# Performance work log

Hardware: AMD Instinct MI355X
Metric: run time of the kernel (lower is better)

Reference implementation:

```python
import jax, jax.numpy as jnp
import numpy as np

N_HEADS = 16
NEG_INF = -1e9


def setup_inputs() -> dict:
    key = jax.random.key(0)
    k1, k2, k3 = jax.random.split(key, 3)
    B, S, D = 4, 4096, 1024
    x = jax.random.normal(k1, (B, S, D), dtype=jnp.float32)
    # GPT-2-style init scale
    w_qkv = jax.random.normal(k2, (D, 3 * D), dtype=jnp.float32) * 0.02
    b_qkv = jnp.zeros((3 * D,), dtype=jnp.float32)
    w_o = jax.random.normal(k3, (D, D), dtype=jnp.float32) * 0.02
    b_o = jnp.zeros((D,), dtype=jnp.float32)
    return {"x": x, "w_qkv": w_qkv, "b_qkv": b_qkv, "w_o": w_o, "b_o": b_o,
            "window_size": 512}


def reference(x, w_qkv, b_qkv, w_o, b_o, window_size):
    B, S, D = x.shape
    W = window_size
    n_win = S // W  # loop `for i in range(0, S, W)` with S % W == 0
    H = N_HEADS
    dh = D // H

    # All windows are independent -> fold them into the batch dim instead of a
    # Python loop (same math as looping + concat along seq dim).
    xw = x.reshape(B * n_win, W, D)

    qkv = xw @ w_qkv + b_qkv                      # [BN, W, 3D]
    q, k, v = jnp.split(qkv, 3, axis=-1)
    # [BN, H, W, dh]
    q = q.reshape(-1, W, H, dh).transpose(0, 2, 1, 3)
    k = k.reshape(-1, W, H, dh).transpose(0, 2, 1, 3)
    v = v.reshape(-1, W, H, dh).transpose(0, 2, 1, 3)

    scale = 1.0 / jnp.sqrt(jnp.asarray(dh, dtype=x.dtype))
    scores = jnp.einsum('bhqd,bhkd->bhqk', q, k) * scale  # [BN, H, W, W]
    causal = jnp.tril(jnp.ones((W, W), dtype=bool))       # GPT-2 causal mask (per window)
    scores = jnp.where(causal, scores, NEG_INF)
    attn = jax.nn.softmax(scores, axis=-1)

    out = jnp.einsum('bhqk,bhkd->bhqd', attn, v)          # [BN, H, W, dh]
    out = out.transpose(0, 2, 1, 3).reshape(-1, W, D)     # [BN, W, D]
    out = out @ w_o + b_o
    return out.reshape(B, S, D)
```

## Files before the change

kernel.cpp:

```cpp
#include <hip/hip_runtime.h>


typedef unsigned short u16;
typedef unsigned int u32;
typedef __attribute__((ext_vector_type(8))) short bf16x8;
typedef __attribute__((ext_vector_type(4))) float f32x4;

__device__ __forceinline__ float bf2f(u16 v) {
  union { u32 u; float f; } t; t.u = ((u32)v) << 16; return t.f;
}
__device__ __forceinline__ u16 f2bf(float f) {
  union { float f; u32 u; } t; t.f = f;
  u32 u = t.u + 0x7fffu + ((t.u >> 16) & 1u);
  return (u16)(u >> 16);
}
__device__ __forceinline__ void g2lds16(const void* g, void* l) {
  __builtin_amdgcn_global_load_lds((const __attribute__((address_space(1))) void*)g,
                                   (__attribute__((address_space(3))) void*)l,
                                   16, 0, 0);
}

__global__ __launch_bounds__(256) void canon_x(
    const float* __restrict__ xf, u16* __restrict__ xb) {
  size_t i = ((size_t)blockIdx.x * 256 + threadIdx.x) * 8;
  float4 a = *(const float4*)(xf + i);
  float4 b = *(const float4*)(xf + i + 4);
  u16 o[8] = { f2bf(a.x), f2bf(a.y), f2bf(a.z), f2bf(a.w),
               f2bf(b.x), f2bf(b.y), f2bf(b.z), f2bf(b.w) };
  *(bf16x8*)(xb + i) = *(bf16x8*)o;
}

__global__ __launch_bounds__(256) void transpose_w(
    const float* __restrict__ in, u16* __restrict__ out, int R, int C) {
  __shared__ u16 tile[32][33];
  int c0 = blockIdx.x * 32, r0 = blockIdx.y * 32;
  int tx = threadIdx.x & 31, ty = threadIdx.x >> 5;
#pragma unroll
  for (int i = 0; i < 32; i += 8)
    tile[ty + i][tx] = f2bf(in[(size_t)(r0 + ty + i) * C + c0 + tx]);
  __syncthreads();
#pragma unroll
  for (int i = 0; i < 32; i += 8)
    out[(size_t)(c0 + ty + i) * R + r0 + tx] = tile[tx][ty + i];
}

__global__ __launch_bounds__(256) void transpose_v(
    const u16* __restrict__ qkv, u16* __restrict__ vt) {
  __shared__ u16 tile[32][33];
  int bh = blockIdx.z, bn = bh >> 4, h = bh & 15;
  int t0 = blockIdx.x * 32, d0 = blockIdx.y * 32;
  int tx = threadIdx.x & 31, ty = threadIdx.x >> 5;
  const u16* src = qkv + (size_t)(bn * 512) * 3072 + 2048 + h * 64;
#pragma unroll
  for (int i = 0; i < 32; i += 8)
    tile[ty + i][tx] = src[(size_t)(t0 + ty + i) * 3072 + d0 + tx];
  __syncthreads();
  u16* dst = vt + ((size_t)bh * 64 + d0) * 512 + t0;
#pragma unroll
  for (int i = 0; i < 32; i += 8)
    dst[(size_t)(ty + i) * 512 + tx] = tile[tx][ty + i];
}

template <typename OutT>
__global__ __launch_bounds__(256, 2) void gemm_bt_bias(
    const u16* __restrict__ A, const u16* __restrict__ Bt,
    const float* __restrict__ bias, OutT* __restrict__ C,
    int M, int N, int K) {
  __shared__ __align__(16) u16 As[128 * 32];
  __shared__ __align__(16) u16 Bs[128 * 32];
  const int tid = threadIdx.x;
  const int wave = tid >> 6, lane = tid & 63;
  const int quad = lane >> 4, l16 = lane & 15;
  const int m0 = blockIdx.y * 128, n0 = blockIdx.x * 128;
  const int wm = (wave >> 1) * 64, wn = (wave & 1) * 64;

  f32x4 acc[4][4] = {};

  int e0 = (wave * 512) + lane * 8;
  int e1 = 2048 + e0;
  int rA0 = e0 >> 5, cA0 = e0 & 31;
  int rA1 = e1 >> 5, cA1 = e1 & 31;
  const u16* ga0 = A + (size_t)(m0 + rA0) * K + cA0;
  const u16* ga1 = A + (size_t)(m0 + rA1) * K + cA1;
  const u16* gb0 = Bt + (size_t)(n0 + rA0) * K + cA0;
  const u16* gb1 = Bt + (size_t)(n0 + rA1) * K + cA1;
  u16* As0 = As + (size_t)wave * 512;
  u16* As1 = As0 + 2048;
  u16* Bs0 = Bs + (size_t)wave * 512;
  u16* Bs1 = Bs0 + 2048;

  for (int k0 = 0; k0 < K; k0 += 32) {
    g2lds16(ga0 + k0, As0);
    g2lds16(ga1 + k0, As1);
    g2lds16(gb0 + k0, Bs0);
    g2lds16(gb1 + k0, Bs1);
    __syncthreads();
    bf16x8 a[4], b[4];
#pragma unroll
    for (int mi = 0; mi < 4; ++mi)
      a[mi] = *(const bf16x8*)(As + (wm + mi * 16 + l16) * 32 + quad * 8);
#pragma unroll
    for (int ni = 0; ni < 4; ++ni)
      b[ni] = *(const bf16x8*)(Bs + (wn + ni * 16 + l16) * 32 + quad * 8);
#pragma unroll
    for (int mi = 0; mi < 4; ++mi)
#pragma unroll
      for (int ni = 0; ni < 4; ++ni)
        acc[mi][ni] = __builtin_amdgcn_mfma_f32_16x16x32_bf16(a[mi], b[ni], acc[mi][ni], 0, 0, 0);
    __syncthreads();
  }

#pragma unroll
  for (int ni = 0; ni < 4; ++ni) {
    int col = n0 + wn + ni * 16 + l16;
    float bv = bias[col];
#pragma unroll
    for (int mi = 0; mi < 4; ++mi) {
      int row = m0 + wm + mi * 16 + quad * 4;
#pragma unroll
      for (int r = 0; r < 4; ++r) {
        float v = acc[mi][ni][r] + bv;
        if constexpr (sizeof(OutT) == 2)
          C[(size_t)(row + r) * N + col] = f2bf(v);
        else
          C[(size_t)(row + r) * N + col] = v;
      }
    }
  }
}

__global__ __launch_bounds__(256, 2) void attn_win(
    const u16* __restrict__ qkv, const u16* __restrict__ vt,
    u16* __restrict__ attn) {
  __shared__ __align__(16) u16 Qs[128 * 64];
  __shared__ __align__(16) u16 Ks[128 * 64];
  __shared__ __align__(16) u16 Vs[64 * 128];
  __shared__ __align__(16) u16 Ps[4][32 * 128];

  const int qt = blockIdx.x, h = blockIdx.y, bn = blockIdx.z;
  const int bh = bn * 16 + h;
  const int tid = threadIdx.x;
  const int wave = tid >> 6, lane = tid & 63;
  const int quad = lane >> 4, l16 = lane & 15;
  const int t0 = bn * 512 + qt * 128;

#pragma unroll
  for (int it = 0; it < 4; ++it) {
    int i = it * 256 + tid;
    int row = i >> 3, c = i & 7;
    bf16x8 v = *(const bf16x8*)(qkv + (size_t)(t0 + row) * 3072 + h * 64 + c * 8);
    *(bf16x8*)(Qs + row * 64 + ((c ^ (row & 7)) * 8)) = v;
  }

  float mrun[2][4], lrun[2][4];
  f32x4 o[2][4] = {};
#pragma unroll
  for (int mi = 0; mi < 2; ++mi)
#pragma unroll
    for (int r = 0; r < 4; ++r) { mrun[mi][r] = -1e30f; lrun[mi][r] = 0.f; }

  const float cexp = 0.18033688011112042f;

  for (int j = 0; j <= qt; ++j) {
    int tk = bn * 512 + j * 128;
#pragma unroll
    for (int it = 0; it < 4; ++it) {
      int i = it * 256 + tid;
      int rk = i >> 3, ck = i & 7;
      bf16x8 kv = *(const bf16x8*)(qkv + (size_t)(tk + rk) * 3072 + 1024 + h * 64 + ck * 8);
      *(bf16x8*)(Ks + rk * 64 + ((ck ^ (rk & 7)) * 8)) = kv;
      int rv = i >> 4, cv = i & 15;
      bf16x8 vv = *(const bf16x8*)(vt + ((size_t)bh * 64 + rv) * 512 + j * 128 + cv * 8);
      *(bf16x8*)(Vs + rv * 128 + ((cv ^ (rv & 15)) * 8)) = vv;
    }
    __syncthreads();

    f32x4 s[2][8] = {};
#pragma unroll
    for (int ks = 0; ks < 2; ++ks) {
      bf16x8 aq[2];
#pragma unroll
      for (int mi = 0; mi < 2; ++mi) {
        int m = wave * 32 + mi * 16 + l16;
        aq[mi] = *(const bf16x8*)(Qs + m * 64 + (((ks * 4 + quad) ^ (m & 7)) * 8));
      }
#pragma unroll
      for (int ni = 0; ni < 8; ++ni) {
        int n = ni * 16 + l16;
        bf16x8 bk = *(const bf16x8*)(Ks + n * 64 + (((ks * 4 + quad) ^ (n & 7)) * 8));
        s[0][ni] = __builtin_amdgcn_mfma_f32_16x16x32_bf16(aq[0], bk, s[0][ni], 0, 0, 0);
        s[1][ni] = __builtin_amdgcn_mfma_f32_16x16x32_bf16(aq[1], bk, s[1][ni], 0, 0, 0);
      }
    }

    const bool diag = (j == qt);
#pragma unroll
    for (int mi = 0; mi < 2; ++mi) {
#pragma unroll
      for (int r = 0; r < 4; ++r) {
        int m = wave * 32 + mi * 16 + quad * 4 + r;
        float rmax = -1e30f;
#pragma unroll
        for (int ni = 0; ni < 8; ++ni) {
          float v = s[mi][ni][r] * cexp;
          if (diag && (ni * 16 + l16 > m)) v = -1e30f;
          s[mi][ni][r] = v;
          rmax = fmaxf(rmax, v);
        }
        rmax = fmaxf(rmax, __shfl_xor(rmax, 1));
        rmax = fmaxf(rmax, __shfl_xor(rmax, 2));
        rmax = fmaxf(rmax, __shfl_xor(rmax, 4));
        rmax = fmaxf(rmax, __shfl_xor(rmax, 8));
        float mnew = fmaxf(mrun[mi][r], rmax);
        float alpha = exp2f(mrun[mi][r] - mnew);
        mrun[mi][r] = mnew;
        float rsum = 0.f;
#pragma unroll
        for (int ni = 0; ni < 8; ++ni) {
          float pv = exp2f(s[mi][ni][r] - mnew);
          s[mi][ni][r] = pv;
          rsum += pv;
        }
        rsum += __shfl_xor(rsum, 1);
        rsum += __shfl_xor(rsum, 2);
        rsum += __shfl_xor(rsum, 4);
        rsum += __shfl_xor(rsum, 8);
        lrun[mi][r] = lrun[mi][r] * alpha + rsum;
#pragma unroll
        for (int di = 0; di < 4; ++di) o[mi][di][r] *= alpha;
      }
    }

    u16* pw = &Ps[wave][0];
#pragma unroll
    for (int mi = 0; mi < 2; ++mi)
#pragma unroll
      for (int ni = 0; ni < 8; ++ni)
#pragma unroll
        for (int r = 0; r < 4; ++r) {
          int row = mi * 16 + quad * 4 + r;
          int col = ni * 16 + l16;
          int phys = (col >> 3) ^ (row & 15);
          pw[row * 128 + phys * 8 + (col & 7)] = f2bf(s[mi][ni][r]);
        }
    __syncthreads();

#pragma unroll
    for (int ks = 0; ks < 4; ++ks) {
      bf16x8 ap[2];
#pragma unroll
      for (int mi = 0; mi < 2; ++mi) {
        int row = mi * 16 + l16;
        ap[mi] = *(const bf16x8*)(pw + row * 128 + (((ks * 4 + quad) ^ (row & 15)) * 8));
      }
#pragma unroll
      for (int di = 0; di < 4; ++di) {
        int n = di * 16 + l16;
        bf16x8 bv = *(const bf16x8*)(Vs + n * 128 + (((ks * 4 + quad) ^ (n & 15)) * 8));
        o[0][di] = __builtin_amdgcn_mfma_f32_16x16x32_bf16(ap[0], bv, o[0][di], 0, 0, 0);
        o[1][di] = __builtin_amdgcn_mfma_f32_16x16x32_bf16(ap[1], bv, o[1][di], 0, 0, 0);
      }
    }
    __syncthreads();
  }

#pragma unroll
  for (int mi = 0; mi < 2; ++mi)
#pragma unroll
    for (int r = 0; r < 4; ++r) {
      float inv = 1.0f / lrun[mi][r];
      int trow = t0 + wave * 32 + mi * 16 + quad * 4 + r;
#pragma unroll
      for (int di = 0; di < 4; ++di)
        attn[(size_t)trow * 1024 + h * 64 + di * 16 + l16] = f2bf(o[mi][di][r] * inv);
    }
}

extern "C" void kernel_launch(void* const* d_in, const int* in_sizes, int n_in,
                              void* d_out, int out_size, void* d_ws, size_t ws_size,
                              hipStream_t stream) {
  (void)in_sizes; (void)n_in; (void)out_size; (void)ws_size;
  const float* x     = (const float*)d_in[0];
  const float* w_qkv = (const float*)d_in[1];
  const float* b_qkv = (const float*)d_in[2];
  const float* w_o   = (const float*)d_in[3];
  const float* b_o   = (const float*)d_in[4];
  float* out = (float*)d_out;

  char* ws = (char*)d_ws;
  u16* qkv   = (u16*)(ws + 0);
  u16* vtb   = (u16*)(ws + 100663296);
  u16* attnb = (u16*)(ws + 134217728);
  u16* xb    = (u16*)(ws + 167772160);
  u16* wqkvT = (u16*)(ws + 201326592);
  u16* woT   = (u16*)(ws + 207618048);

  canon_x<<<8192, 256, 0, stream>>>(x, xb);
  transpose_w<<<dim3(96, 32), 256, 0, stream>>>(w_qkv, wqkvT, 1024, 3072);
  transpose_w<<<dim3(32, 32), 256, 0, stream>>>(w_o, woT, 1024, 1024);

  gemm_bt_bias<u16><<<dim3(24, 128), 256, 0, stream>>>(
      xb, wqkvT, b_qkv, qkv, 16384, 3072, 1024);
  transpose_v<<<dim3(16, 2, 512), 256, 0, stream>>>(qkv, vtb);
  attn_win<<<dim3(4, 16, 32), 256, 0, stream>>>(qkv, vtb, attnb);
  gemm_bt_bias<float><<<dim3(8, 128), 256, 0, stream>>>(
      attnb, woT, b_o, out, 16384, 1024, 1024);
}
```

Baseline: 468.3 us.

## Load attention Q/K/V operands straight from global into registers, dropping LDS staging

The windowed attention kernel no longer stages Q, K and V tiles in shared memory. Each wave loads its Q fragments into registers once and reads K and V MFMA operands directly from global memory on every step. Because only the per-wave P buffer stays in LDS, the block-wide barriers are removed. The smaller LDS footprint lets the launch bound rise to 3 blocks per CU, and s_setprio is raised around the MFMA loops. In exchange, every wave re-fetches the same K/V tiles, which multiplies L2/global traffic and exposes load latency next to the MFMAs.

```diff
diff --git a/kernel.cpp b/kernel.cpp
--- a/kernel.cpp
+++ b/kernel.cpp
@@ -129,12 +129,9 @@
   }
 }
 
-__global__ __launch_bounds__(256, 2) void attn_win(
+__global__ __launch_bounds__(256, 3) void attn_win(
     const u16* __restrict__ qkv, const u16* __restrict__ vt,
     u16* __restrict__ attn) {
-  __shared__ __align__(16) u16 Qs[128 * 64];
-  __shared__ __align__(16) u16 Ks[128 * 64];
-  __shared__ __align__(16) u16 Vs[64 * 128];
   __shared__ __align__(16) u16 Ps[4][32 * 128];
 
   const int qt = blockIdx.x, h = blockIdx.y, bn = blockIdx.z;
@@ -144,13 +141,13 @@
   const int quad = lane >> 4, l16 = lane & 15;
   const int t0 = bn * 512 + qt * 128;
 
-#pragma unroll
-  for (int it = 0; it < 4; ++it) {
-    int i = it * 256 + tid;
-    int row = i >> 3, c = i & 7;
-    bf16x8 v = *(const bf16x8*)(qkv + (size_t)(t0 + row) * 3072 + h * 64 + c * 8);
-    *(bf16x8*)(Qs + row * 64 + ((c ^ (row & 7)) * 8)) = v;
-  }
+  bf16x8 aq[2][2];
+#pragma unroll
+  for (int mi = 0; mi < 2; ++mi)
+#pragma unroll
+    for (int ks = 0; ks < 2; ++ks)
+      aq[mi][ks] = *(const bf16x8*)(
+          qkv + (size_t)(t0 + wave * 32 + mi * 16 + l16) * 3072 + h * 64 + ks * 32 + quad * 8);
 
   float mrun[2][4], lrun[2][4];
   f32x4 o[2][4] = {};
@@ -161,37 +158,26 @@
 
   const float cexp = 0.18033688011112042f;
 
+  const u16* Kb = qkv + 1024 + h * 64;
+  const u16* Vb = vt + (size_t)bh * 64 * 512;
+  u16* pw = &Ps[wave][0];
+
   for (int j = 0; j <= qt; ++j) {
-    int tk = bn * 512 + j * 128;
-#pragma unroll
-    for (int it = 0; it < 4; ++it) {
-      int i = it * 256 + tid;
-      int rk = i >> 3, ck = i & 7;
-      bf16x8 kv = *(const bf16x8*)(qkv + (size_t)(tk + rk) * 3072 + 1024 + h * 64 + ck * 8);
-      *(bf16x8*)(Ks + rk * 64 + ((ck ^ (rk & 7)) * 8)) = kv;
-      int rv = i >> 4, cv = i & 15;
-      bf16x8 vv = *(const bf16x8*)(vt + ((size_t)bh * 64 + rv) * 512 + j * 128 + cv * 8);
-      *(bf16x8*)(Vs + rv * 128 + ((cv ^ (rv & 15)) * 8)) = vv;
-    }
-    __syncthreads();
+    const int tk = bn * 512 + j * 128;
 
     f32x4 s[2][8] = {};
+    __builtin_amdgcn_s_setprio(1);
 #pragma unroll
     for (int ks = 0; ks < 2; ++ks) {
-      bf16x8 aq[2];
-#pragma unroll
-      for (int mi = 0; mi < 2; ++mi) {
-        int m = wave * 32 + mi * 16 + l16;
-        aq[mi] = *(const bf16x8*)(Qs + m * 64 + (((ks * 4 + quad) ^ (m & 7)) * 8));
-      }
 #pragma unroll
       for (int ni = 0; ni < 8; ++ni) {
-        int n = ni * 16 + l16;
-        bf16x8 bk = *(const bf16x8*)(Ks + n * 64 + (((ks * 4 + quad) ^ (n & 7)) * 8));
-        s[0][ni] = __builtin_amdgcn_mfma_f32_16x16x32_bf16(aq[0], bk, s[0][ni], 0, 0, 0);
-        s[1][ni] = __builtin_amdgcn_mfma_f32_16x16x32_bf16(aq[1], bk, s[1][ni], 0, 0, 0);
-      }
-    }
+        bf16x8 bk = *(const bf16x8*)(
+            Kb + (size_t)(tk + ni * 16 + l16) * 3072 + ks * 32 + quad * 8);
+        s[0][ni] = __builtin_amdgcn_mfma_f32_16x16x32_bf16(aq[0][ks], bk, s[0][ni], 0, 0, 0);
+        s[1][ni] = __builtin_amdgcn_mfma_f32_16x16x32_bf16(aq[1][ks], bk, s[1][ni], 0, 0, 0);
+      }
+    }
+    __builtin_amdgcn_s_setprio(0);
 
     const bool diag = (j == qt);
 #pragma unroll
@@ -231,7 +217,6 @@
       }
     }
 
-    u16* pw = &Ps[wave][0];
 #pragma unroll
     for (int mi = 0; mi < 2; ++mi)
 #pragma unroll
@@ -243,8 +228,8 @@
           int phys = (col >> 3) ^ (row & 15);
           pw[row * 128 + phys * 8 + (col & 7)] = f2bf(s[mi][ni][r]);
         }
-    __syncthreads();
-
+
+    __builtin_amdgcn_s_setprio(1);
 #pragma unroll
     for (int ks = 0; ks < 4; ++ks) {
       bf16x8 ap[2];
@@ -255,13 +240,13 @@
       }
 #pragma unroll
       for (int di = 0; di < 4; ++di) {
-        int n = di * 16 + l16;
-        bf16x8 bv = *(const bf16x8*)(Vs + n * 128 + (((ks * 4 + quad) ^ (n & 15)) * 8));
+        bf16x8 bv = *(const bf16x8*)(
+            Vb + (size_t)(di * 16 + l16) * 512 + j * 128 + ks * 32 + quad * 8);
         o[0][di] = __builtin_amdgcn_mfma_f32_16x16x32_bf16(ap[0], bv, o[0][di], 0, 0, 0);
         o[1][di] = __builtin_amdgcn_mfma_f32_16x16x32_bf16(ap[1], bv, o[1][di], 0, 0, 0);
       }
     }
-    __syncthreads();
+    __builtin_amdgcn_s_setprio(0);
   }
 
 #pragma unroll
```

After: 683.8 us. 1.46x slower.

## Keep Q in registers, prefetch next K/V tile, halve P buffer for occupancy

Applied to the files above, without the earlier changes.

The attention kernel now loads Q fragments straight into registers instead of staging them through shared memory. It prefetches the next K/V tile into registers while the PV MFMAs of the current tile run, then writes that tile to LDS between two barriers. The P staging buffer is halved by processing the two 16-row halves one after the other, and launch bounds are raised to 3 blocks per CU. s_setprio raises wave priority around the MFMA sections. The extra register pressure from holding Q, K and V in registers may cause spills or block the higher occupancy target.

```diff
diff --git a/kernel.cpp b/kernel.cpp
--- a/kernel.cpp
+++ b/kernel.cpp
@@ -129,13 +129,12 @@
   }
 }
 
-__global__ __launch_bounds__(256, 2) void attn_win(
+__global__ __launch_bounds__(256, 3) void attn_win(
     const u16* __restrict__ qkv, const u16* __restrict__ vt,
     u16* __restrict__ attn) {
-  __shared__ __align__(16) u16 Qs[128 * 64];
   __shared__ __align__(16) u16 Ks[128 * 64];
   __shared__ __align__(16) u16 Vs[64 * 128];
-  __shared__ __align__(16) u16 Ps[4][32 * 128];
+  __shared__ __align__(16) u16 Ps[4][16 * 128];
 
   const int qt = blockIdx.x, h = blockIdx.y, bn = blockIdx.z;
   const int bh = bn * 16 + h;
@@ -144,25 +143,16 @@
   const int quad = lane >> 4, l16 = lane & 15;
   const int t0 = bn * 512 + qt * 128;
 
-#pragma unroll
-  for (int it = 0; it < 4; ++it) {
-    int i = it * 256 + tid;
-    int row = i >> 3, c = i & 7;
-    bf16x8 v = *(const bf16x8*)(qkv + (size_t)(t0 + row) * 3072 + h * 64 + c * 8);
-    *(bf16x8*)(Qs + row * 64 + ((c ^ (row & 7)) * 8)) = v;
-  }
-
-  float mrun[2][4], lrun[2][4];
-  f32x4 o[2][4] = {};
+  bf16x8 aq[2][2];
 #pragma unroll
   for (int mi = 0; mi < 2; ++mi)
 #pragma unroll
-    for (int r = 0; r < 4; ++r) { mrun[mi][r] = -1e30f; lrun[mi][r] = 0.f; }
-
-  const float cexp = 0.18033688011112042f;
-
-  for (int j = 0; j <= qt; ++j) {
-    int tk = bn * 512 + j * 128;
+    for (int ks = 0; ks < 2; ++ks)
+      aq[mi][ks] = *(const bf16x8*)(
+          qkv + (size_t)(t0 + wave * 32 + mi * 16 + l16) * 3072 + h * 64 + ks * 32 + quad * 8);
+
+  {
+    const int tk = bn * 512;
 #pragma unroll
     for (int it = 0; it < 4; ++it) {
       int i = it * 256 + tid;
@@ -170,28 +160,38 @@
       bf16x8 kv = *(const bf16x8*)(qkv + (size_t)(tk + rk) * 3072 + 1024 + h * 64 + ck * 8);
       *(bf16x8*)(Ks + rk * 64 + ((ck ^ (rk & 7)) * 8)) = kv;
       int rv = i >> 4, cv = i & 15;
-      bf16x8 vv = *(const bf16x8*)(vt + ((size_t)bh * 64 + rv) * 512 + j * 128 + cv * 8);
+      bf16x8 vv = *(const bf16x8*)(vt + ((size_t)bh * 64 + rv) * 512 + cv * 8);
       *(bf16x8*)(Vs + rv * 128 + ((cv ^ (rv & 15)) * 8)) = vv;
     }
-    __syncthreads();
-
+  }
+  __syncthreads();
+
+  float mrun[2][4], lrun[2][4];
+  f32x4 o[2][4] = {};
+#pragma unroll
+  for (int mi = 0; mi < 2; ++mi)
+#pragma unroll
+    for (int r = 0; r < 4; ++r) { mrun[mi][r] = -1e30f; lrun[mi][r] = 0.f; }
+
+  const float cexp = 0.18033688011112042f;
+
+  bf16x8 kreg[4], vreg[4];
+  u16* pw = &Ps[wave][0];
+
+  for (int j = 0; j <= qt; ++j) {
     f32x4 s[2][8] = {};
+    __builtin_amdgcn_s_setprio(1);
 #pragma unroll
     for (int ks = 0; ks < 2; ++ks) {
-      bf16x8 aq[2];
-#pragma unroll
-      for (int mi = 0; mi < 2; ++mi) {
-        int m = wave * 32 + mi * 16 + l16;
-        aq[mi] = *(const bf16x8*)(Qs + m * 64 + (((ks * 4 + quad) ^ (m & 7)) * 8));
-      }
 #pragma unroll
       for (int ni = 0; ni < 8; ++ni) {
         int n = ni * 16 + l16;
         bf16x8 bk = *(const bf16x8*)(Ks + n * 64 + (((ks * 4 + quad) ^ (n & 7)) * 8));
-        s[0][ni] = __builtin_amdgcn_mfma_f32_16x16x32_bf16(aq[0], bk, s[0][ni], 0, 0, 0);
-        s[1][ni] = __builtin_amdgcn_mfma_f32_16x16x32_bf16(aq[1], bk, s[1][ni], 0, 0, 0);
-      }
-    }
+        s[0][ni] = __builtin_amdgcn_mfma_f32_16x16x32_bf16(aq[0][ks], bk, s[0][ni], 0, 0, 0);
+        s[1][ni] = __builtin_amdgcn_mfma_f32_16x16x32_bf16(aq[1][ks], bk, s[1][ni], 0, 0, 0);
+      }
+    }
+    __builtin_amdgcn_s_setprio(0);
 
     const bool diag = (j == qt);
 #pragma unroll
@@ -231,37 +231,78 @@
       }
     }
 
-    u16* pw = &Ps[wave][0];
-#pragma unroll
-    for (int mi = 0; mi < 2; ++mi)
-#pragma unroll
-      for (int ni = 0; ni < 8; ++ni)
-#pragma unroll
-        for (int r = 0; r < 4; ++r) {
-          int row = mi * 16 + quad * 4 + r;
-          int col = ni * 16 + l16;
-          int phys = (col >> 3) ^ (row & 15);
-          pw[row * 128 + phys * 8 + (col & 7)] = f2bf(s[mi][ni][r]);
-        }
-    __syncthreads();
-
-#pragma unroll
-    for (int ks = 0; ks < 4; ++ks) {
-      bf16x8 ap[2];
-#pragma unroll
-      for (int mi = 0; mi < 2; ++mi) {
-        int row = mi * 16 + l16;
-        ap[mi] = *(const bf16x8*)(pw + row * 128 + (((ks * 4 + quad) ^ (row & 15)) * 8));
-      }
+#pragma unroll
+    for (int ni = 0; ni < 8; ++ni)
+#pragma unroll
+      for (int r = 0; r < 4; ++r) {
+        int row = quad * 4 + r;
+        int col = ni * 16 + l16;
+        int phys = (col >> 3) ^ row;
+        pw[row * 128 + phys * 8 + (col & 7)] = f2bf(s[0][ni][r]);
+      }
+
+    __builtin_amdgcn_s_setprio(1);
+#pragma unroll
+    for (int ksv = 0; ksv < 4; ++ksv) {
+      bf16x8 ap = *(const bf16x8*)(pw + l16 * 128 + (((ksv * 4 + quad) ^ l16) * 8));
 #pragma unroll
       for (int di = 0; di < 4; ++di) {
         int n = di * 16 + l16;
-        bf16x8 bv = *(const bf16x8*)(Vs + n * 128 + (((ks * 4 + quad) ^ (n & 15)) * 8));
-        o[0][di] = __builtin_amdgcn_mfma_f32_16x16x32_bf16(ap[0], bv, o[0][di], 0, 0, 0);
-        o[1][di] = __builtin_amdgcn_mfma_f32_16x16x32_bf16(ap[1], bv, o[1][di], 0, 0, 0);
-      }
-    }
-    __syncthreads();
+        bf16x8 bv = *(const bf16x8*)(Vs + n * 128 + (((ksv * 4 + quad) ^ (n & 15)) * 8));
+        o[0][di] = __builtin_amdgcn_mfma_f32_16x16x32_bf16(ap, bv, o[0][di], 0, 0, 0);
+      }
+    }
+    __builtin_amdgcn_s_setprio(0);
+
+    if (j < qt) {
+      const int tk1 = bn * 512 + (j + 1) * 128;
+#pragma unroll
+      for (int it = 0; it < 4; ++it) {
+        int i = it * 256 + tid;
+        int rk = i >> 3, ck = i & 7;
+        kreg[it] = *(const bf16x8*)(
+            qkv + (size_t)(tk1 + rk) * 3072 + 1024 + h * 64 + ck * 8);
+        int rv = i >> 4, cv = i & 15;
+        vreg[it] = *(const bf16x8*)(
+            vt + ((size_t)bh * 64 + rv) * 512 + (j + 1) * 128 + cv * 8);
+      }
+    }
+
+#pragma unroll
+    for (int ni = 0; ni < 8; ++ni)
+#pragma unroll
+      for (int r = 0; r < 4; ++r) {
+        int row = quad * 4 + r;
+        int col = ni * 16 + l16;
+        int phys = (col >> 3) ^ row;
+        pw[row * 128 + phys * 8 + (col & 7)] = f2bf(s[1][ni][r]);
+      }
+
+    __builtin_amdgcn_s_setprio(1);
+#pragma unroll
+    for (int ksv = 0; ksv < 4; ++ksv) {
+      bf16x8 ap = *(const bf16x8*)(pw + l16 * 128 + (((ksv * 4 + quad) ^ l16) * 8));
+#pragma unroll
+      for (int di = 0; di < 4; ++di) {
+        int n = di * 16 + l16;
+        bf16x8 bv = *(const bf16x8*)(Vs + n * 128 + (((ksv * 4 + quad) ^ (n & 15)) * 8));
+        o[1][di] = __builtin_amdgcn_mfma_f32_16x16x32_bf16(ap, bv, o[1][di], 0, 0, 0);
+      }
+    }
+    __builtin_amdgcn_s_setprio(0);
+
+    if (j < qt) {
+      __syncthreads();
+#pragma unroll
+      for (int it = 0; it < 4; ++it) {
+        int i = it * 256 + tid;
+        int rk = i >> 3, ck = i & 7;
+        *(bf16x8*)(Ks + rk * 64 + ((ck ^ (rk & 7)) * 8)) = kreg[it];
+        int rv = i >> 4, cv = i & 15;
+        *(bf16x8*)(Vs + rv * 128 + ((cv ^ (rv & 15)) * 8)) = vreg[it];
+      }
+      __syncthreads();
+    }
   }
 
 #pragma unroll
```

After: 606.8 us. 1.3x slower.
